# Performance work log

Hardware: AMD Instinct MI355X
Metric: run time of the kernel (lower is better)

The kernel has to match this reference:

```python
import jax, jax.numpy as jnp
import numpy as np

NUM_CLASSES = 81
HIDDEN_DIM = 1024
N_ROIS = 4096
SAMPLE = 7
FEAT = 256
FEATURE_DIM = SAMPLE * SAMPLE * FEAT  # 12544


def setup_inputs() -> dict:
    key = jax.random.key(0)
    k_feat, k_idx, k1, k2, k3 = jax.random.split(key, 5)
    features = jax.random.normal(k_feat, (N_ROIS, SAMPLE, SAMPLE, FEAT), dtype=jnp.float32)
    batch_indices = jnp.sort(jax.random.randint(k_idx, (N_ROIS,), 0, 8, dtype=jnp.int32))
    # Glorot-uniform init like keras Dense defaults; zero biases.
    def glorot(k, fan_in, fan_out):
        lim = np.sqrt(6.0 / (fan_in + fan_out)).astype(np.float32)
        return jax.random.uniform(k, (fan_in, fan_out), dtype=jnp.float32, minval=-lim, maxval=lim)
    w1 = glorot(k1, FEATURE_DIM, HIDDEN_DIM)
    b1 = jnp.zeros((HIDDEN_DIM,), jnp.float32)
    w2 = glorot(k2, HIDDEN_DIM, HIDDEN_DIM)
    b2 = jnp.zeros((HIDDEN_DIM,), jnp.float32)
    w3 = glorot(k3, HIDDEN_DIM, NUM_CLASSES * 4)
    b3 = jnp.zeros((NUM_CLASSES * 4,), jnp.float32)
    return {"features": features, "batch_indices": batch_indices,
            "w1": w1, "b1": b1, "w2": w2, "b2": b2, "w3": w3, "b3": b3}


def reference(features, batch_indices, w1, b1, w2, b2, w3, b3):
    # The TF module gathers rows per image, runs the shared MLP, then
    # scatters results back into original row order via argsort of the
    # concatenated indices. Because the MLP weights are shared across
    # images, the permutation and its inverse cancel: the result equals
    # the MLP applied row-wise to the flattened features in-place.
    # batch_indices only determines the (identity-composed) permutation.
    n = features.shape[0]
    x = features.reshape(n, -1)                 # [N, 12544]
    x = jax.nn.relu(x @ w1 + b1)                # [N, 1024]
    x = jax.nn.relu(x @ w2 + b2)                # [N, 1024]
    bbox_deltas = x @ w3 + b3                   # [N, num_classes*4]
    return bbox_deltas
```

## Files before the change

kernel.cpp:

```cpp
#include <hip/hip_runtime.h>


typedef __attribute__((ext_vector_type(4)))  float          f32x4;
typedef __attribute__((ext_vector_type(8)))  short          short8;
typedef __attribute__((ext_vector_type(4)))  unsigned int   uint4v;
typedef __attribute__((ext_vector_type(4)))  unsigned short ushort4v;
typedef __attribute__((ext_vector_type(8)))  unsigned short ushort8v;

#define BM 128
#define BN 128
#define BK 64

__device__ __forceinline__ void split_f32(float x, unsigned short& h, unsigned short& l) {
    unsigned int u = __float_as_uint(x);
    h = (unsigned short)(u >> 16);
    float hf = __uint_as_float(u & 0xFFFF0000u);
    l = (unsigned short)(__float_as_uint(x - hf) >> 16);
}

__global__ __launch_bounds__(256) void convert_w_t(const float* __restrict__ W,
                                                   unsigned short* __restrict__ WhT,
                                                   unsigned short* __restrict__ WlT,
                                                   int K, int N) {
    __shared__ float tile[64][65];
    const int k0 = blockIdx.y * 64;
    const int n0 = blockIdx.x * 64;
    const int tid = threadIdx.x;
    const int kr = tid >> 4;
    const int nc = (tid & 15) * 4;
#pragma unroll
    for (int i = 0; i < 4; ++i) {
        const int k = kr + 16 * i;
        f32x4 v = (f32x4){0.f, 0.f, 0.f, 0.f};
        if (n0 + nc < N) v = *(const f32x4*)(W + (size_t)(k0 + k) * N + n0 + nc);
        tile[k][nc + 0] = v[0];
        tile[k][nc + 1] = v[1];
        tile[k][nc + 2] = v[2];
        tile[k][nc + 3] = v[3];
    }
    __syncthreads();
    const int nr = tid >> 2;
    const int kc = (tid & 3) * 16;
    ushort8v h0, h1, l0, l1;
#pragma unroll
    for (int j = 0; j < 8; ++j) {
        unsigned short hh, ll;
        split_f32(tile[kc + j][nr], hh, ll);
        h0[j] = hh; l0[j] = ll;
        split_f32(tile[kc + 8 + j][nr], hh, ll);
        h1[j] = hh; l1[j] = ll;
    }
    const size_t o = (size_t)(n0 + nr) * K + k0 + kc;
    *(ushort8v*)(WhT + o)     = h0;
    *(ushort8v*)(WhT + o + 8) = h1;
    *(ushort8v*)(WlT + o)     = l0;
    *(ushort8v*)(WlT + o + 8) = l1;
}

template<bool A_F32, int EPI>
__global__ __launch_bounds__(256, 2)
void gemm3split(const float* __restrict__ A32,
                const unsigned short* __restrict__ Ah,
                const unsigned short* __restrict__ Al,
                const unsigned short* __restrict__ BhT,
                const unsigned short* __restrict__ BlT,
                const float* __restrict__ bias,
                unsigned short* __restrict__ Ch,
                unsigned short* __restrict__ Cl,
                float* __restrict__ Cf,
                int K, int ktiles, int ldC) {
    const int tid  = threadIdx.x;
    const int lane = tid & 63;
    const int wave = tid >> 6;
    const int kgrp = lane >> 4;
    const int m0 = blockIdx.x * BM;
    const int n0 = blockIdx.y * BN;
    const int kt_base = blockIdx.z * ktiles;
    const int wm = (wave >> 1) * 64;
    const int wn = (wave & 1) * 64;

    __shared__ __align__(16) unsigned short sAh[BM * BK];
    __shared__ __align__(16) unsigned short sAl[BM * BK];
    __shared__ __align__(16) unsigned short sBh[BN * BK];
    __shared__ __align__(16) unsigned short sBl[BN * BK];

    f32x4 acc[4][4];
#pragma unroll
    for (int m = 0; m < 4; ++m)
#pragma unroll
        for (int n = 0; n < 4; ++n) acc[m][n] = (f32x4){0.f, 0.f, 0.f, 0.f};

    const int arow   = tid >> 4;
    const int acol4  = tid & 15;
    const int brow   = tid >> 3;
    const int bchunk = tid & 7;

    f32x4  aF[8];
    uint4v aH[4], aL[4];
    uint4v bH[4], bL[4];

    auto load_tile = [&](int kt) {
        const int k0 = (kt_base + kt) * BK;
        if constexpr (A_F32) {
#pragma unroll
            for (int i = 0; i < 8; ++i)
                aF[i] = *(const f32x4*)(A32 + (size_t)(m0 + arow + 16 * i) * K + k0 + acol4 * 4);
        } else {
#pragma unroll
            for (int i = 0; i < 4; ++i) {
                const size_t off = (size_t)(m0 + brow + 32 * i) * K + k0 + bchunk * 8;
                aH[i] = *(const uint4v*)(Ah + off);
                aL[i] = *(const uint4v*)(Al + off);
            }
        }
#pragma unroll
        for (int i = 0; i < 4; ++i) {
            const size_t off = (size_t)(n0 + brow + 32 * i) * K + k0 + bchunk * 8;
            bH[i] = *(const uint4v*)(BhT + off);
            bL[i] = *(const uint4v*)(BlT + off);
        }
    };

    auto stage_to_lds = [&]() {
        if constexpr (A_F32) {
#pragma unroll
            for (int i = 0; i < 8; ++i) {
                const int r = arow + 16 * i;
                ushort4v h, l;
#pragma unroll
                for (int j = 0; j < 4; ++j) {
                    unsigned short hh, ll;
                    split_f32(aF[i][j], hh, ll);
                    h[j] = hh; l[j] = ll;
                }
                const int ck  = acol4 >> 1;
                const int sub = (acol4 & 1) * 4;
                const int off = r * BK + ((ck ^ (r & 7)) << 3) + sub;
                *(ushort4v*)(sAh + off) = h;
                *(ushort4v*)(sAl + off) = l;
            }
        } else {
#pragma unroll
            for (int i = 0; i < 4; ++i) {
                const int r   = brow + 32 * i;
                const int off = r * BK + ((bchunk ^ (r & 7)) << 3);
                *(uint4v*)(sAh + off) = aH[i];
                *(uint4v*)(sAl + off) = aL[i];
            }
        }
#pragma unroll
        for (int i = 0; i < 4; ++i) {
            const int r   = brow + 32 * i;
            const int off = r * BK + ((bchunk ^ (r & 7)) << 3);
            *(uint4v*)(sBh + off) = bH[i];
            *(uint4v*)(sBl + off) = bL[i];
        }
    };

    load_tile(0);

    for (int kt = 0; kt < ktiles; ++kt) {
        __syncthreads();
        stage_to_lds();
        __syncthreads();
        if (kt + 1 < ktiles) load_tile(kt + 1);
#pragma unroll
        for (int kk = 0; kk < BK / 32; ++kk) {
            const int ck = kk * 4 + kgrp;
            short8 fah[4], fal[4];
#pragma unroll
            for (int m = 0; m < 4; ++m) {
                const int r   = wm + m * 16 + (lane & 15);
                const int off = r * BK + ((ck ^ (r & 7)) << 3);
                fah[m] = *(const short8*)(sAh + off);
                fal[m] = *(const short8*)(sAl + off);
            }
#pragma unroll
            for (int n = 0; n < 4; ++n) {
                const int r   = wn + n * 16 + (lane & 15);
                const int off = r * BK + ((ck ^ (r & 7)) << 3);
                const short8 fbh = *(const short8*)(sBh + off);
                const short8 fbl = *(const short8*)(sBl + off);
#pragma unroll
                for (int m = 0; m < 4; ++m) {
                    acc[m][n] = __builtin_amdgcn_mfma_f32_16x16x32_bf16(fah[m], fbh, acc[m][n], 0, 0, 0);
                    acc[m][n] = __builtin_amdgcn_mfma_f32_16x16x32_bf16(fah[m], fbl, acc[m][n], 0, 0, 0);
                    acc[m][n] = __builtin_amdgcn_mfma_f32_16x16x32_bf16(fal[m], fbh, acc[m][n], 0, 0, 0);
                }
            }
        }
    }

    const int col  = lane & 15;
    const int row4 = (lane >> 4) * 4;
#pragma unroll
    for (int n = 0; n < 4; ++n) {
        const int gn = n0 + wn + n * 16 + col;
        if constexpr (EPI == 0) {
            const float bv = bias[gn];
#pragma unroll
            for (int m = 0; m < 4; ++m) {
                const int gmb = m0 + wm + m * 16 + row4;
#pragma unroll
                for (int j = 0; j < 4; ++j) {
                    float v = acc[m][n][j] + bv;
                    v = fmaxf(v, 0.0f);
                    unsigned short hh, ll;
                    split_f32(v, hh, ll);
                    const size_t o = (size_t)(gmb + j) * ldC + gn;
                    Ch[o] = hh;
                    Cl[o] = ll;
                }
            }
        } else {
            float* Cp = Cf + (size_t)blockIdx.z * (size_t)gridDim.x * BM * ldC;
#pragma unroll
            for (int m = 0; m < 4; ++m) {
                const int gmb = m0 + wm + m * 16 + row4;
#pragma unroll
                for (int j = 0; j < 4; ++j) {
                    Cp[(size_t)(gmb + j) * ldC + gn] = acc[m][n][j];
                }
            }
        }
    }
}

__global__ __launch_bounds__(256) void reduce_relu_split(
        const float* __restrict__ P, size_t planeStride, int nplanes,
        const float* __restrict__ bias, int ldmask,
        unsigned short* __restrict__ Ch, unsigned short* __restrict__ Cl) {
    const size_t base = ((size_t)blockIdx.x * 256 + threadIdx.x) * 4;
    f32x4 s = *(const f32x4*)(P + base);
    for (int z = 1; z < nplanes; ++z)
        s += *(const f32x4*)(P + (size_t)z * planeStride + base);
    const int colb = (int)(base & (size_t)ldmask);
    const f32x4 b = *(const f32x4*)(bias + colb);
    ushort4v h, l;
#pragma unroll
    for (int j = 0; j < 4; ++j) {
        float v = fmaxf(s[j] + b[j], 0.0f);
        unsigned short hh, ll;
        split_f32(v, hh, ll);
        h[j] = hh; l[j] = ll;
    }
    *(ushort4v*)(Ch + base) = h;
    *(ushort4v*)(Cl + base) = l;
}

__global__ __launch_bounds__(128) void reduce_bias_out(
        const float* __restrict__ P, const float* __restrict__ bias,
        float* __restrict__ out) {
    const int col = blockIdx.x * 128 + threadIdx.x;
    const int row = blockIdx.y;
    if (col >= 324) return;
    float s = bias[col];
#pragma unroll
    for (int z = 0; z < 4; ++z)
        s += P[((size_t)z * 4096 + row) * 384 + col];
    out[(size_t)row * 324 + col] = s;
}

static constexpr size_t SZ_W1P  = (size_t)1024 * 12544 * 2;
static constexpr size_t SZ_W2P  = (size_t)1024 * 1024  * 2;
static constexpr size_t SZ_W3P  = (size_t)384  * 1024  * 2;
static constexpr size_t SZ_P    = (size_t)2 * 4096 * 1024 * 4;
static constexpr size_t SZ_CP   = (size_t)4096 * 1024 * 2;
static constexpr size_t OFF_W1H = 0;
static constexpr size_t OFF_W1L = OFF_W1H + SZ_W1P;
static constexpr size_t OFF_W2H = OFF_W1L + SZ_W1P;
static constexpr size_t OFF_W2L = OFF_W2H + SZ_W2P;
static constexpr size_t OFF_W3H = OFF_W2L + SZ_W2P;
static constexpr size_t OFF_W3L = OFF_W3H + SZ_W3P;
static constexpr size_t OFF_P   = OFF_W3L + SZ_W3P;
static constexpr size_t WS_NEED = OFF_P + SZ_P;
static constexpr size_t OFF_C1H = OFF_W1H;
static constexpr size_t OFF_C1L = OFF_W1H + SZ_CP;
static constexpr size_t OFF_C2H = OFF_W1L;
static constexpr size_t OFF_C2L = OFF_W1L + SZ_CP;

extern "C" void kernel_launch(void* const* d_in, const int* in_sizes, int n_in,
                              void* d_out, int out_size, void* d_ws, size_t ws_size,
                              hipStream_t stream) {
    const float* features = (const float*)d_in[0];
    const float* w1 = (const float*)d_in[2];
    const float* b1 = (const float*)d_in[3];
    const float* w2 = (const float*)d_in[4];
    const float* b2 = (const float*)d_in[5];
    const float* w3 = (const float*)d_in[6];
    const float* b3 = (const float*)d_in[7];
    float* out = (float*)d_out;

    if (ws_size < WS_NEED) return;

    char* ws = (char*)d_ws;
    unsigned short* W1h = (unsigned short*)(ws + OFF_W1H);
    unsigned short* W1l = (unsigned short*)(ws + OFF_W1L);
    unsigned short* W2h = (unsigned short*)(ws + OFF_W2H);
    unsigned short* W2l = (unsigned short*)(ws + OFF_W2L);
    unsigned short* W3h = (unsigned short*)(ws + OFF_W3H);
    unsigned short* W3l = (unsigned short*)(ws + OFF_W3L);
    unsigned short* C1h = (unsigned short*)(ws + OFF_C1H);
    unsigned short* C1l = (unsigned short*)(ws + OFF_C1L);
    unsigned short* C2h = (unsigned short*)(ws + OFF_C2H);
    unsigned short* C2l = (unsigned short*)(ws + OFF_C2L);
    float*          P   = (float*)(ws + OFF_P);

    convert_w_t<<<dim3(1024 / 64, 12544 / 64), 256, 0, stream>>>(w1, W1h, W1l, 12544, 1024);
    convert_w_t<<<dim3(1024 / 64, 1024  / 64), 256, 0, stream>>>(w2, W2h, W2l, 1024, 1024);
    convert_w_t<<<dim3(384  / 64, 1024  / 64), 256, 0, stream>>>(w3, W3h, W3l, 1024, 324);

    gemm3split<true, 1><<<dim3(4096 / BM, 1024 / BN, 2), 256, 0, stream>>>(
        features, nullptr, nullptr, W1h, W1l, nullptr, nullptr, nullptr, P,
        12544, 98, 1024);
    reduce_relu_split<<<4096, 256, 0, stream>>>(
        P, (size_t)4096 * 1024, 2, b1, 1023, C1h, C1l);

    gemm3split<false, 0><<<dim3(4096 / BM, 1024 / BN, 1), 256, 0, stream>>>(
        nullptr, C1h, C1l, W2h, W2l, b2, C2h, C2l, nullptr,
        1024, 16, 1024);

    gemm3split<false, 1><<<dim3(4096 / BM, 384 / BN, 4), 256, 0, stream>>>(
        nullptr, C2h, C2l, W3h, W3l, nullptr, nullptr, nullptr, P,
        1024, 4, 384);
    reduce_bias_out<<<dim3(3, 4096), 128, 0, stream>>>(P, b3, out);
}
```

Before: 635.2 us.

## Template K-tile size and raise split-K for layers one and two

Makes the GEMM K-tile size a template parameter, with launch bounds of 4 blocks per CU when the K-tile is 32. When the workspace allows it, layer one runs with BK=32 and split-K of 4 instead of BK=64 and split-K of 2, giving more blocks and higher occupancy from the smaller LDS footprint. Layer two switches from a fused bias/ReLU epilogue to split-K 2 plus a separate reduce kernel, adding parallelism for 256 blocks. The cost is extra partial-sum traffic, extra reduce passes and a larger workspace requirement.

```diff
diff --git a/kernel.cpp b/kernel.cpp
--- a/kernel.cpp
+++ b/kernel.cpp
@@ -9,7 +9,6 @@
 
 #define BM 128
 #define BN 128
-#define BK 64
 
 __device__ __forceinline__ void split_f32(float x, unsigned short& h, unsigned short& l) {
     unsigned int u = __float_as_uint(x);
@@ -57,8 +56,8 @@
     *(ushort8v*)(WlT + o + 8) = l1;
 }
 
-template<bool A_F32, int EPI>
-__global__ __launch_bounds__(256, 2)
+template<bool A_F32, int EPI, int BKT>
+__global__ __launch_bounds__(256, BKT == 32 ? 4 : 2)
 void gemm3split(const float* __restrict__ A32,
                 const unsigned short* __restrict__ Ah,
                 const unsigned short* __restrict__ Al,
@@ -69,6 +68,14 @@
                 unsigned short* __restrict__ Cl,
                 float* __restrict__ Cf,
                 int K, int ktiles, int ldC) {
+    constexpr int CHUNKS = BKT / 8;
+    constexpr int XM     = CHUNKS - 1;
+    constexpr int F4     = BKT / 4;
+    constexpr int AROWS  = 256 / F4;
+    constexpr int AIT    = BM / AROWS;
+    constexpr int BROWS  = 256 / CHUNKS;
+    constexpr int BIT    = BM / BROWS;
+
     const int tid  = threadIdx.x;
     const int lane = tid & 63;
     const int wave = tid >> 6;
@@ -79,10 +86,10 @@
     const int wm = (wave >> 1) * 64;
     const int wn = (wave & 1) * 64;
 
-    __shared__ __align__(16) unsigned short sAh[BM * BK];
-    __shared__ __align__(16) unsigned short sAl[BM * BK];
-    __shared__ __align__(16) unsigned short sBh[BN * BK];
-    __shared__ __align__(16) unsigned short sBl[BN * BK];
+    __shared__ __align__(16) unsigned short sAh[BM * BKT];
+    __shared__ __align__(16) unsigned short sAl[BM * BKT];
+    __shared__ __align__(16) unsigned short sBh[BN * BKT];
+    __shared__ __align__(16) unsigned short sBl[BN * BKT];
 
     f32x4 acc[4][4];
 #pragma unroll
@@ -90,32 +97,32 @@
 #pragma unroll
         for (int n = 0; n < 4; ++n) acc[m][n] = (f32x4){0.f, 0.f, 0.f, 0.f};
 
-    const int arow   = tid >> 4;
-    const int acol4  = tid & 15;
-    const int brow   = tid >> 3;
-    const int bchunk = tid & 7;
-
-    f32x4  aF[8];
-    uint4v aH[4], aL[4];
-    uint4v bH[4], bL[4];
+    const int arow   = tid / F4;
+    const int acol4  = tid % F4;
+    const int brow   = tid / CHUNKS;
+    const int bchunk = tid % CHUNKS;
+
+    f32x4  aF[AIT];
+    uint4v aH[BIT], aL[BIT];
+    uint4v bH[BIT], bL[BIT];
 
     auto load_tile = [&](int kt) {
-        const int k0 = (kt_base + kt) * BK;
+        const int k0 = (kt_base + kt) * BKT;
         if constexpr (A_F32) {
 #pragma unroll
-            for (int i = 0; i < 8; ++i)
-                aF[i] = *(const f32x4*)(A32 + (size_t)(m0 + arow + 16 * i) * K + k0 + acol4 * 4);
+            for (int i = 0; i < AIT; ++i)
+                aF[i] = *(const f32x4*)(A32 + (size_t)(m0 + arow + AROWS * i) * K + k0 + acol4 * 4);
         } else {
 #pragma unroll
-            for (int i = 0; i < 4; ++i) {
-                const size_t off = (size_t)(m0 + brow + 32 * i) * K + k0 + bchunk * 8;
+            for (int i = 0; i < BIT; ++i) {
+                const size_t off = (size_t)(m0 + brow + BROWS * i) * K + k0 + bchunk * 8;
                 aH[i] = *(const uint4v*)(Ah + off);
                 aL[i] = *(const uint4v*)(Al + off);
             }
         }
 #pragma unroll
-        for (int i = 0; i < 4; ++i) {
-            const size_t off = (size_t)(n0 + brow + 32 * i) * K + k0 + bchunk * 8;
+        for (int i = 0; i < BIT; ++i) {
+            const size_t off = (size_t)(n0 + brow + BROWS * i) * K + k0 + bchunk * 8;
             bH[i] = *(const uint4v*)(BhT + off);
             bL[i] = *(const uint4v*)(BlT + off);
         }
@@ -124,8 +131,8 @@
     auto stage_to_lds = [&]() {
         if constexpr (A_F32) {
 #pragma unroll
-            for (int i = 0; i < 8; ++i) {
-                const int r = arow + 16 * i;
+            for (int i = 0; i < AIT; ++i) {
+                const int r = arow + AROWS * i;
                 ushort4v h, l;
 #pragma unroll
                 for (int j = 0; j < 4; ++j) {
@@ -135,23 +142,23 @@
                 }
                 const int ck  = acol4 >> 1;
                 const int sub = (acol4 & 1) * 4;
-                const int off = r * BK + ((ck ^ (r & 7)) << 3) + sub;
+                const int off = r * BKT + ((ck ^ (r & XM)) << 3) + sub;
                 *(ushort4v*)(sAh + off) = h;
                 *(ushort4v*)(sAl + off) = l;
             }
         } else {
 #pragma unroll
-            for (int i = 0; i < 4; ++i) {
-                const int r   = brow + 32 * i;
-                const int off = r * BK + ((bchunk ^ (r & 7)) << 3);
+            for (int i = 0; i < BIT; ++i) {
+                const int r   = brow + BROWS * i;
+                const int off = r * BKT + ((bchunk ^ (r & XM)) << 3);
                 *(uint4v*)(sAh + off) = aH[i];
                 *(uint4v*)(sAl + off) = aL[i];
             }
         }
 #pragma unroll
-        for (int i = 0; i < 4; ++i) {
-            const int r   = brow + 32 * i;
-            const int off = r * BK + ((bchunk ^ (r & 7)) << 3);
+        for (int i = 0; i < BIT; ++i) {
+            const int r   = brow + BROWS * i;
+            const int off = r * BKT + ((bchunk ^ (r & XM)) << 3);
             *(uint4v*)(sBh + off) = bH[i];
             *(uint4v*)(sBl + off) = bL[i];
         }
@@ -165,20 +172,20 @@
         __syncthreads();
         if (kt + 1 < ktiles) load_tile(kt + 1);
 #pragma unroll
-        for (int kk = 0; kk < BK / 32; ++kk) {
+        for (int kk = 0; kk < BKT / 32; ++kk) {
             const int ck = kk * 4 + kgrp;
             short8 fah[4], fal[4];
 #pragma unroll
             for (int m = 0; m < 4; ++m) {
                 const int r   = wm + m * 16 + (lane & 15);
-                const int off = r * BK + ((ck ^ (r & 7)) << 3);
+                const int off = r * BKT + ((ck ^ (r & XM)) << 3);
                 fah[m] = *(const short8*)(sAh + off);
                 fal[m] = *(const short8*)(sAl + off);
             }
 #pragma unroll
             for (int n = 0; n < 4; ++n) {
                 const int r   = wn + n * 16 + (lane & 15);
-                const int off = r * BK + ((ck ^ (r & 7)) << 3);
+                const int off = r * BKT + ((ck ^ (r & XM)) << 3);
                 const short8 fbh = *(const short8*)(sBh + off);
                 const short8 fbl = *(const short8*)(sBl + off);
 #pragma unroll
@@ -264,7 +271,7 @@
 static constexpr size_t SZ_W1P  = (size_t)1024 * 12544 * 2;
 static constexpr size_t SZ_W2P  = (size_t)1024 * 1024  * 2;
 static constexpr size_t SZ_W3P  = (size_t)384  * 1024  * 2;
-static constexpr size_t SZ_P    = (size_t)2 * 4096 * 1024 * 4;
+static constexpr size_t SZ_PLANE= (size_t)4096 * 1024 * 4;
 static constexpr size_t SZ_CP   = (size_t)4096 * 1024 * 2;
 static constexpr size_t OFF_W1H = 0;
 static constexpr size_t OFF_W1L = OFF_W1H + SZ_W1P;
@@ -273,7 +280,8 @@
 static constexpr size_t OFF_W3H = OFF_W2L + SZ_W2P;
 static constexpr size_t OFF_W3L = OFF_W3H + SZ_W3P;
 static constexpr size_t OFF_P   = OFF_W3L + SZ_W3P;
-static constexpr size_t WS_NEED = OFF_P + SZ_P;
+static constexpr size_t WS_SMALL = OFF_P + 2 * SZ_PLANE;
+static constexpr size_t WS_BIG   = OFF_P + 4 * SZ_PLANE;
 static constexpr size_t OFF_C1H = OFF_W1H;
 static constexpr size_t OFF_C1L = OFF_W1H + SZ_CP;
 static constexpr size_t OFF_C2H = OFF_W1L;
@@ -291,7 +299,8 @@
     const float* b3 = (const float*)d_in[7];
     float* out = (float*)d_out;
 
-    if (ws_size < WS_NEED) return;
+    if (ws_size < WS_SMALL) return;
+    const bool big = (ws_size >= WS_BIG);
 
     char* ws = (char*)d_ws;
     unsigned short* W1h = (unsigned short*)(ws + OFF_W1H);
@@ -310,17 +319,27 @@
     convert_w_t<<<dim3(1024 / 64, 1024  / 64), 256, 0, stream>>>(w2, W2h, W2l, 1024, 1024);
     convert_w_t<<<dim3(384  / 64, 1024  / 64), 256, 0, stream>>>(w3, W3h, W3l, 1024, 324);
 
-    gemm3split<true, 1><<<dim3(4096 / BM, 1024 / BN, 2), 256, 0, stream>>>(
-        features, nullptr, nullptr, W1h, W1l, nullptr, nullptr, nullptr, P,
-        12544, 98, 1024);
+    if (big) {
+        gemm3split<true, 1, 32><<<dim3(4096 / BM, 1024 / BN, 4), 256, 0, stream>>>(
+            features, nullptr, nullptr, W1h, W1l, nullptr, nullptr, nullptr, P,
+            12544, 98, 1024);
+        reduce_relu_split<<<4096, 256, 0, stream>>>(
+            P, (size_t)4096 * 1024, 4, b1, 1023, C1h, C1l);
+    } else {
+        gemm3split<true, 1, 64><<<dim3(4096 / BM, 1024 / BN, 2), 256, 0, stream>>>(
+            features, nullptr, nullptr, W1h, W1l, nullptr, nullptr, nullptr, P,
+            12544, 98, 1024);
+        reduce_relu_split<<<4096, 256, 0, stream>>>(
+            P, (size_t)4096 * 1024, 2, b1, 1023, C1h, C1l);
+    }
+
+    gemm3split<false, 1, 64><<<dim3(4096 / BM, 1024 / BN, 2), 256, 0, stream>>>(
+        nullptr, C1h, C1l, W2h, W2l, nullptr, nullptr, nullptr, P,
+        1024, 8, 1024);
     reduce_relu_split<<<4096, 256, 0, stream>>>(
-        P, (size_t)4096 * 1024, 2, b1, 1023, C1h, C1l);
-
-    gemm3split<false, 0><<<dim3(4096 / BM, 1024 / BN, 1), 256, 0, stream>>>(
-        nullptr, C1h, C1l, W2h, W2l, b2, C2h, C2l, nullptr,
-        1024, 16, 1024);
-
-    gemm3split<false, 1><<<dim3(4096 / BM, 384 / BN, 4), 256, 0, stream>>>(
+        P, (size_t)4096 * 1024, 2, b2, 1023, C2h, C2l);
+
+    gemm3split<false, 1, 64><<<dim3(4096 / BM, 384 / BN, 4), 256, 0, stream>>>(
         nullptr, C2h, C2l, W3h, W3l, nullptr, nullptr, nullptr, P,
         1024, 4, 384);
     reduce_bias_out<<<dim3(3, 4096), 128, 0, stream>>>(P, b3, out);
```

New measurement: 1.572 ms. 148% more time.

## Fuse split-K reduction, bias and ReLU into next GEMM's A-operand load

Applied to the files above, without the earlier changes.

Removes the reduce_relu_split kernel and the bf16 hi/lo activation buffers. Each following GEMM now reads both fp32 split-K partial planes directly, sums them, adds the bias, applies ReLU and splits to hi/lo while staging into LDS. The second GEMM switches to split-K=2 and writes fp32 partials instead of bf16 pairs. This saves a launch and a write/read round trip, but the A operand traffic doubles (two fp32 planes per element) and the partial sums are recomputed by every N-tile block.

```diff
diff --git a/kernel.cpp b/kernel.cpp
--- a/kernel.cpp
+++ b/kernel.cpp
@@ -57,16 +57,13 @@
     *(ushort8v*)(WlT + o + 8) = l1;
 }
 
-template<bool A_F32, int EPI>
+template<int ASRC>
 __global__ __launch_bounds__(256, 2)
-void gemm3split(const float* __restrict__ A32,
-                const unsigned short* __restrict__ Ah,
-                const unsigned short* __restrict__ Al,
+void gemm3split(const float* __restrict__ A0,
+                const float* __restrict__ A1,
+                const float* __restrict__ abias,
                 const unsigned short* __restrict__ BhT,
                 const unsigned short* __restrict__ BlT,
-                const float* __restrict__ bias,
-                unsigned short* __restrict__ Ch,
-                unsigned short* __restrict__ Cl,
                 float* __restrict__ Cf,
                 int K, int ktiles, int ldC) {
     const int tid  = threadIdx.x;
@@ -96,23 +93,19 @@
     const int bchunk = tid & 7;
 
     f32x4  aF[8];
-    uint4v aH[4], aL[4];
+    f32x4  aG[8];
+    f32x4  aB;
     uint4v bH[4], bL[4];
 
     auto load_tile = [&](int kt) {
         const int k0 = (kt_base + kt) * BK;
-        if constexpr (A_F32) {
-#pragma unroll
-            for (int i = 0; i < 8; ++i)
-                aF[i] = *(const f32x4*)(A32 + (size_t)(m0 + arow + 16 * i) * K + k0 + acol4 * 4);
-        } else {
-#pragma unroll
-            for (int i = 0; i < 4; ++i) {
-                const size_t off = (size_t)(m0 + brow + 32 * i) * K + k0 + bchunk * 8;
-                aH[i] = *(const uint4v*)(Ah + off);
-                aL[i] = *(const uint4v*)(Al + off);
-            }
-        }
+#pragma unroll
+        for (int i = 0; i < 8; ++i) {
+            const size_t off = (size_t)(m0 + arow + 16 * i) * K + k0 + acol4 * 4;
+            aF[i] = *(const f32x4*)(A0 + off);
+            if constexpr (ASRC == 1) aG[i] = *(const f32x4*)(A1 + off);
+        }
+        if constexpr (ASRC == 1) aB = *(const f32x4*)(abias + k0 + acol4 * 4);
 #pragma unroll
         for (int i = 0; i < 4; ++i) {
             const size_t off = (size_t)(n0 + brow + 32 * i) * K + k0 + bchunk * 8;
@@ -122,31 +115,23 @@
     };
 
     auto stage_to_lds = [&]() {
-        if constexpr (A_F32) {
-#pragma unroll
-            for (int i = 0; i < 8; ++i) {
-                const int r = arow + 16 * i;
-                ushort4v h, l;
-#pragma unroll
-                for (int j = 0; j < 4; ++j) {
-                    unsigned short hh, ll;
-                    split_f32(aF[i][j], hh, ll);
-                    h[j] = hh; l[j] = ll;
-                }
-                const int ck  = acol4 >> 1;
-                const int sub = (acol4 & 1) * 4;
-                const int off = r * BK + ((ck ^ (r & 7)) << 3) + sub;
-                *(ushort4v*)(sAh + off) = h;
-                *(ushort4v*)(sAl + off) = l;
-            }
-        } else {
-#pragma unroll
-            for (int i = 0; i < 4; ++i) {
-                const int r   = brow + 32 * i;
-                const int off = r * BK + ((bchunk ^ (r & 7)) << 3);
-                *(uint4v*)(sAh + off) = aH[i];
-                *(uint4v*)(sAl + off) = aL[i];
-            }
+#pragma unroll
+        for (int i = 0; i < 8; ++i) {
+            const int r = arow + 16 * i;
+            ushort4v h, l;
+#pragma unroll
+            for (int j = 0; j < 4; ++j) {
+                float v = aF[i][j];
+                if constexpr (ASRC == 1) v = fmaxf(v + aG[i][j] + aB[j], 0.0f);
+                unsigned short hh, ll;
+                split_f32(v, hh, ll);
+                h[j] = hh; l[j] = ll;
+            }
+            const int ck  = acol4 >> 1;
+            const int sub = (acol4 & 1) * 4;
+            const int off = r * BK + ((ck ^ (r & 7)) << 3) + sub;
+            *(ushort4v*)(sAh + off) = h;
+            *(ushort4v*)(sAl + off) = l;
         }
 #pragma unroll
         for (int i = 0; i < 4; ++i) {
@@ -193,59 +178,19 @@
 
     const int col  = lane & 15;
     const int row4 = (lane >> 4) * 4;
+    float* Cp = Cf + (size_t)blockIdx.z * (size_t)gridDim.x * BM * ldC;
 #pragma unroll
     for (int n = 0; n < 4; ++n) {
         const int gn = n0 + wn + n * 16 + col;
-        if constexpr (EPI == 0) {
-            const float bv = bias[gn];
-#pragma unroll
-            for (int m = 0; m < 4; ++m) {
-                const int gmb = m0 + wm + m * 16 + row4;
-#pragma unroll
-                for (int j = 0; j < 4; ++j) {
-                    float v = acc[m][n][j] + bv;
-                    v = fmaxf(v, 0.0f);
-                    unsigned short hh, ll;
-                    split_f32(v, hh, ll);
-                    const size_t o = (size_t)(gmb + j) * ldC + gn;
-                    Ch[o] = hh;
-                    Cl[o] = ll;
-                }
-            }
-        } else {
-            float* Cp = Cf + (size_t)blockIdx.z * (size_t)gridDim.x * BM * ldC;
-#pragma unroll
-            for (int m = 0; m < 4; ++m) {
-                const int gmb = m0 + wm + m * 16 + row4;
-#pragma unroll
-                for (int j = 0; j < 4; ++j) {
-                    Cp[(size_t)(gmb + j) * ldC + gn] = acc[m][n][j];
-                }
-            }
-        }
-    }
-}
-
-__global__ __launch_bounds__(256) void reduce_relu_split(
-        const float* __restrict__ P, size_t planeStride, int nplanes,
-        const float* __restrict__ bias, int ldmask,
-        unsigned short* __restrict__ Ch, unsigned short* __restrict__ Cl) {
-    const size_t base = ((size_t)blockIdx.x * 256 + threadIdx.x) * 4;
-    f32x4 s = *(const f32x4*)(P + base);
-    for (int z = 1; z < nplanes; ++z)
-        s += *(const f32x4*)(P + (size_t)z * planeStride + base);
-    const int colb = (int)(base & (size_t)ldmask);
-    const f32x4 b = *(const f32x4*)(bias + colb);
-    ushort4v h, l;
-#pragma unroll
-    for (int j = 0; j < 4; ++j) {
-        float v = fmaxf(s[j] + b[j], 0.0f);
-        unsigned short hh, ll;
-        split_f32(v, hh, ll);
-        h[j] = hh; l[j] = ll;
-    }
-    *(ushort4v*)(Ch + base) = h;
-    *(ushort4v*)(Cl + base) = l;
+#pragma unroll
+        for (int m = 0; m < 4; ++m) {
+            const int gmb = m0 + wm + m * 16 + row4;
+#pragma unroll
+            for (int j = 0; j < 4; ++j) {
+                Cp[(size_t)(gmb + j) * ldC + gn] = acc[m][n][j];
+            }
+        }
+    }
 }
 
 __global__ __launch_bounds__(128) void reduce_bias_out(
@@ -261,23 +206,20 @@
     out[(size_t)row * 324 + col] = s;
 }
 
-static constexpr size_t SZ_W1P  = (size_t)1024 * 12544 * 2;
-static constexpr size_t SZ_W2P  = (size_t)1024 * 1024  * 2;
-static constexpr size_t SZ_W3P  = (size_t)384  * 1024  * 2;
-static constexpr size_t SZ_P    = (size_t)2 * 4096 * 1024 * 4;
-static constexpr size_t SZ_CP   = (size_t)4096 * 1024 * 2;
-static constexpr size_t OFF_W1H = 0;
-static constexpr size_t OFF_W1L = OFF_W1H + SZ_W1P;
-static constexpr size_t OFF_W2H = OFF_W1L + SZ_W1P;
-static constexpr size_t OFF_W2L = OFF_W2H + SZ_W2P;
-static constexpr size_t OFF_W3H = OFF_W2L + SZ_W2P;
-static constexpr size_t OFF_W3L = OFF_W3H + SZ_W3P;
-static constexpr size_t OFF_P   = OFF_W3L + SZ_W3P;
-static constexpr size_t WS_NEED = OFF_P + SZ_P;
-static constexpr size_t OFF_C1H = OFF_W1H;
-static constexpr size_t OFF_C1L = OFF_W1H + SZ_CP;
-static constexpr size_t OFF_C2H = OFF_W1L;
-static constexpr size_t OFF_C2L = OFF_W1L + SZ_CP;
+static constexpr size_t SZ_W1P   = (size_t)1024 * 12544 * 2;
+static constexpr size_t SZ_W2P   = (size_t)1024 * 1024  * 2;
+static constexpr size_t SZ_W3P   = (size_t)384  * 1024  * 2;
+static constexpr size_t SZ_PLANE = (size_t)4096 * 1024 * 4;
+static constexpr size_t OFF_W1H  = 0;
+static constexpr size_t OFF_W1L  = OFF_W1H + SZ_W1P;
+static constexpr size_t OFF_W2H  = OFF_W1L + SZ_W1P;
+static constexpr size_t OFF_W2L  = OFF_W2H + SZ_W2P;
+static constexpr size_t OFF_W3H  = OFF_W2L + SZ_W2P;
+static constexpr size_t OFF_W3L  = OFF_W3H + SZ_W3P;
+static constexpr size_t OFF_P1   = OFF_W3L + SZ_W3P;
+static constexpr size_t OFF_P2   = OFF_P1 + 2 * SZ_PLANE;
+static constexpr size_t WS_NEED  = OFF_P2 + 2 * SZ_PLANE;
+static constexpr size_t OFF_P3   = OFF_P1;
 
 extern "C" void kernel_launch(void* const* d_in, const int* in_sizes, int n_in,
                               void* d_out, int out_size, void* d_ws, size_t ws_size,
@@ -300,28 +242,23 @@
     unsigned short* W2l = (unsigned short*)(ws + OFF_W2L);
     unsigned short* W3h = (unsigned short*)(ws + OFF_W3H);
     unsigned short* W3l = (unsigned short*)(ws + OFF_W3L);
-    unsigned short* C1h = (unsigned short*)(ws + OFF_C1H);
-    unsigned short* C1l = (unsigned short*)(ws + OFF_C1L);
-    unsigned short* C2h = (unsigned short*)(ws + OFF_C2H);
-    unsigned short* C2l = (unsigned short*)(ws + OFF_C2L);
-    float*          P   = (float*)(ws + OFF_P);
+    float*          P1  = (float*)(ws + OFF_P1);
+    float*          P2  = (float*)(ws + OFF_P2);
+    float*          P3  = (float*)(ws + OFF_P3);
+    const size_t PS = (size_t)4096 * 1024;
 
     convert_w_t<<<dim3(1024 / 64, 12544 / 64), 256, 0, stream>>>(w1, W1h, W1l, 12544, 1024);
     convert_w_t<<<dim3(1024 / 64, 1024  / 64), 256, 0, stream>>>(w2, W2h, W2l, 1024, 1024);
     convert_w_t<<<dim3(384  / 64, 1024  / 64), 256, 0, stream>>>(w3, W3h, W3l, 1024, 324);
 
-    gemm3split<true, 1><<<dim3(4096 / BM, 1024 / BN, 2), 256, 0, stream>>>(
-        features, nullptr, nullptr, W1h, W1l, nullptr, nullptr, nullptr, P,
-        12544, 98, 1024);
-    reduce_relu_split<<<4096, 256, 0, stream>>>(
-        P, (size_t)4096 * 1024, 2, b1, 1023, C1h, C1l);
-
-    gemm3split<false, 0><<<dim3(4096 / BM, 1024 / BN, 1), 256, 0, stream>>>(
-        nullptr, C1h, C1l, W2h, W2l, b2, C2h, C2l, nullptr,
-        1024, 16, 1024);
-
-    gemm3split<false, 1><<<dim3(4096 / BM, 384 / BN, 4), 256, 0, stream>>>(
-        nullptr, C2h, C2l, W3h, W3l, nullptr, nullptr, nullptr, P,
-        1024, 4, 384);
-    reduce_bias_out<<<dim3(3, 4096), 128, 0, stream>>>(P, b3, out);
-}
+    gemm3split<0><<<dim3(4096 / BM, 1024 / BN, 2), 256, 0, stream>>>(
+        features, nullptr, nullptr, W1h, W1l, P1, 12544, 98, 1024);
+
+    gemm3split<1><<<dim3(4096 / BM, 1024 / BN, 2), 256, 0, stream>>>(
+        P1, P1 + PS, b1, W2h, W2l, P2, 1024, 8, 1024);
+
+    gemm3split<1><<<dim3(4096 / BM, 384 / BN, 4), 256, 0, stream>>>(
+        P2, P2 + PS, b2, W3h, W3l, P3, 1024, 4, 384);
+
+    reduce_bias_out<<<dim3(3, 4096), 128, 0, stream>>>(P3, b3, out);
+}
```

New measurement: 625.7 us. About the same (-1.5%).
